# Optimization experiments

Measured on AMD Instinct MI355X. Metric: run time of the kernel, lower is better.

The kernel has to match this reference:

```python
import jax, jax.numpy as jnp
import numpy as np

N = 16384
D = 512
K = 1024          # fixed num_clusters (torch code uses randint(2, N//2))
NUM_ITERS = 10    # kmeans Lloyd iterations
NUM_CLUSTER_ITERS = 1
TEMPERATURE = 0.1
CONCENTRATION = 0.1
EPS = 1e-6


def setup_inputs() -> dict:
    key = jax.random.key(0)
    feats = jax.random.normal(key, (N, D), dtype=jnp.float32)
    return {"feats": feats}


def _assign(feats, centroids, x_sq):
    c_sq = jnp.sum(centroids * centroids, axis=-1)            # [K]
    d = x_sq[:, None] - 2.0 * (feats @ centroids.T) + c_sq[None, :]
    return jnp.argmin(d, axis=-1)                             # [N] int32


def _kmeans(feats, num_clusters, num_iters):
    x_sq = jnp.sum(feats * feats, axis=-1)                    # [N]
    init_centroids = feats[:num_clusters]                     # deterministic init

    def body(_, centroids):
        clusters = _assign(feats, centroids, x_sq)
        sums = jax.ops.segment_sum(feats, clusters, num_segments=num_clusters)
        counts = jax.ops.segment_sum(jnp.ones((feats.shape[0],), feats.dtype),
                                     clusters, num_segments=num_clusters)
        new_c = sums / jnp.maximum(counts, 1.0)[:, None]
        # keep old centroid for empty clusters
        return jnp.where(counts[:, None] > 0, new_c, centroids)

    centroids = jax.lax.fori_loop(0, num_iters, body, init_centroids)
    clusters = _assign(feats, centroids, x_sq)
    counts = jax.ops.segment_sum(jnp.ones((feats.shape[0],), feats.dtype),
                                 clusters, num_segments=num_clusters)
    return clusters, centroids, counts


def reference(feats):
    clusters, centroids, _ = _kmeans(feats, K, NUM_ITERS)
    # per-point squared residuals gathered by cluster id, scatter-added to [K, D]
    resid2 = (feats - centroids[clusters]) ** 2               # [N, D]
    dists = jax.ops.segment_sum(resid2, clusters, num_segments=K)  # [K, D]
    # entropy loss branch (concentration phi)
    p = jnp.exp(-dists / CONCENTRATION)
    Q = p / jnp.sum(p)
    entropy = jnp.mean(Q * jnp.log(Q + EPS)) / NUM_CLUSTER_ITERS
    # nll branch (temperature t)
    p2 = jnp.exp(-dists / TEMPERATURE)
    nll = -jnp.mean(jnp.log(p2 + EPS))
    return entropy + nll
```

## Files before the change

### kernel.cpp

```cpp
#include <hip/hip_runtime.h>
#include <math.h>

#define N 16384
#define D 512
#define K 1024
#define NUM_ITERS 10
#define TEMPERATURE 0.1f
#define CONCENTRATION 0.1f
#define EPS 1e-6f

typedef unsigned short ushort_t;
typedef unsigned int uint_t;
typedef unsigned long long u64;
typedef __attribute__((ext_vector_type(4))) float floatx4;
typedef __attribute__((ext_vector_type(8))) short shortx8;

__device__ inline ushort_t f2h(float f) {
    _Float16 h = (_Float16)f;
    return *(ushort_t*)&h;
}

__device__ inline unsigned ford(float f) {
    unsigned b = __float_as_uint(f);
    return (b & 0x80000000u) ? ~b : (b | 0x80000000u);
}

__device__ inline void f4add(float4& a, const float4& b) {
    a.x += b.x; a.y += b.y; a.z += b.z; a.w += b.w;
}

__device__ inline void gld16(const void* g, void* l) {
    __builtin_amdgcn_global_load_lds(
        (const __attribute__((address_space(1))) void*)(uintptr_t)(g),
        (__attribute__((address_space(3))) void*)(uintptr_t)(l), 16, 0, 0);
}

#define WAITVM(n_lit) asm volatile("s_waitcnt vmcnt(" #n_lit ")" ::: "memory")

__global__ void split_kernel(const float* __restrict__ x, ushort_t* __restrict__ hi,
                             u64* __restrict__ best2, int n4) {
    int i = blockIdx.x * 256 + threadIdx.x;
    if (i >= n4) return;
    float4 v = ((const float4*)x)[i];
    ushort4 hv = {f2h(v.x), f2h(v.y), f2h(v.z), f2h(v.w)};
    ((ushort4*)hi)[i] = hv;
    if (i < 2 * N) best2[i] = ~0ull;
}

__global__ void rowsq_kernel(const float* __restrict__ x, float* __restrict__ out, int rows) {
    int row = blockIdx.x * 4 + (threadIdx.x >> 6);
    int lane = threadIdx.x & 63;
    if (row >= rows) return;
    const float* r = x + (size_t)row * D;
    float s = 0.f;
    for (int i = lane; i < D; i += 64) { float v = r[i]; s += v * v; }
    for (int off = 32; off > 0; off >>= 1) s += __shfl_down(s, off, 64);
    if (lane == 0) out[row] = s;
}

__global__ __launch_bounds__(512, 2) void assign_mfma2(
    const ushort_t* __restrict__ Ah, const ushort_t* __restrict__ Bh,
    const float* __restrict__ csq, u64* __restrict__ best)
{
    __shared__ __align__(16) ushort_t sA[4][8192];
    __shared__ __align__(16) ushort_t sB[4][8192];

    const int tid = threadIdx.x;
    const int lane = tid & 63;
    const int wave = tid >> 6;
    const int wr = wave >> 2, wc = wave & 3;
    const int quad = lane >> 4, l16 = lane & 15;

    const int bid = (int)blockIdx.x;
    const int xid = bid & 7;
    const int s = bid >> 3;
    const int brow = (xid << 3) + (s >> 2);
    const int bcol = s & 3;
    const int row0 = brow * 256, col0 = bcol * 256;

    floatx4 acc[8][4];
#pragma unroll
    for (int a = 0; a < 8; ++a)
#pragma unroll
        for (int b = 0; b < 4; ++b) acc[a][b] = (floatx4){0.f, 0.f, 0.f, 0.f};

    const int swz = (quad ^ (l16 & 3) ^ ((l16 >> 2) & 3)) * 8;
    const int aoff = (wr * 128 + l16) * 32 + swz;
    const int boff = (wc * 64 + l16) * 32 + swz;

    auto stage = [&](int h) {
        const int u_h = h >> 2;
        const int part = h & 3;
        const int kh = part >> 1;
        const int reg = ((u_h & 1) << 1) | kh;
        const int d_off = u_h * 64 + kh * 32;
        const ushort_t* src = (part & 1) ? Bh : Ah;
        const int r0 = (part & 1) ? col0 : row0;
        ushort_t* dstreg = (part & 1) ? &sB[reg][0] : &sA[reg][0];
#pragma unroll
        for (int ii = 0; ii < 2; ++ii) {
            const int idx = ii * 512 + tid;
            const int row = idx >> 2;
            const int kb = (idx & 3) ^ (row & 3) ^ ((row >> 2) & 3);
            gld16(src + (size_t)(r0 + row) * D + d_off + kb * 8, dstreg + idx * 8);
        }
    };

    #pragma unroll
    for (int h = 0; h < 6; ++h) stage(h);
    WAITVM(8);
    __builtin_amdgcn_s_barrier();
    __builtin_amdgcn_sched_barrier(0);

    shortx8 fb[4];
#pragma unroll
    for (int u = 0; u < 8; ++u) {
        const int rbase = (u & 1) << 1;
#pragma unroll
        for (int p = 0; p < 4; ++p) {
            const int g = u * 4 + p;
            if (g + 6 < 32) stage(g + 6);
            const int kh = p >> 1;
            const int ih = p & 1;
            const ushort_t* Areg = &sA[rbase + kh][0];
            const ushort_t* Breg = &sB[rbase + kh][0];
            shortx8 fa[4];
            if (ih == 0) {
#pragma unroll
                for (int j = 0; j < 4; ++j) fb[j] = *(const shortx8*)&Breg[boff + j * 512];
            }
#pragma unroll
            for (int i = 0; i < 4; ++i) fa[i] = *(const shortx8*)&Areg[aoff + (ih * 4 + i) * 512];
            __builtin_amdgcn_s_setprio(1);
#pragma unroll
            for (int i = 0; i < 4; ++i)
#pragma unroll
                for (int j = 0; j < 4; ++j)
                    acc[ih * 4 + i][j] = __builtin_amdgcn_mfma_f32_16x16x32_f16(
                        fa[i], fb[j], acc[ih * 4 + i][j], 0, 0, 0);
            __builtin_amdgcn_s_setprio(0);
            if ((p == 1 || p == 3) && !(u == 7 && p == 3)) {
                asm volatile("s_waitcnt lgkmcnt(0)" ::: "memory");
                if (u == 7 && p == 1)      { WAITVM(0); }
                else if (u == 6 && p == 3) { WAITVM(4); }
                else                       { WAITVM(8); }
                __builtin_amdgcn_s_barrier();
                __builtin_amdgcn_sched_barrier(0);
            }
        }
    }

    float csqv[4];
#pragma unroll
    for (int j = 0; j < 4; ++j) csqv[j] = csq[col0 + wc * 64 + j * 16 + l16];

    const int k0 = col0 + wc * 64 + l16;
#pragma unroll
    for (int i = 0; i < 8; ++i) {
#pragma unroll
        for (int r = 0; r < 4; ++r) {
            float bv = csqv[0] - 2.0f * acc[i][0][r];
            int bk = k0;
#pragma unroll
            for (int j = 1; j < 4; ++j) {
                float v = csqv[j] - 2.0f * acc[i][j][r];
                int kk = k0 + j * 16;
                if (v < bv || (v == bv && kk < bk)) { bv = v; bk = kk; }
            }
#pragma unroll
            for (int m = 1; m < 16; m <<= 1) {
                float ov = __shfl_xor(bv, m, 64);
                int ok = __shfl_xor(bk, m, 64);
                if (ov < bv || (ov == bv && ok < bk)) { bv = ov; bk = ok; }
            }
            if (l16 == 0) {
                int p = row0 + wr * 128 + i * 16 + quad * 4 + r;
                u64 pk = ((u64)ford(bv) << 32) | (unsigned)bk;
                atomicMin(&best[p], pk);
            }
        }
    }
}

#define CU_WAVES 8
#define CHUNKS (N / 128)
#define ROUNDS 4
#define WIN (CHUNKS / ROUNDS)
#define CPW (WIN / CU_WAVES)
#define KPB 2

__global__ __launch_bounds__(512) void cluster_update(
    const float* __restrict__ feats, const u64* __restrict__ best,
    u64* __restrict__ best_other,
    float* __restrict__ cent, ushort_t* __restrict__ Bh,
    float* __restrict__ csq)
{
    __shared__ int list[KPB][CU_WAVES][CPW * 128];
    __shared__ int lcnt[KPB][CU_WAVES];
    __shared__ float4 part[CU_WAVES][64][2];
    __shared__ int pcnt_s[CU_WAVES];

    const int tid = threadIdx.x;
    const int lane = tid & 63;
    const int wave = tid >> 6;
    const int kbase = (int)blockIdx.x * KPB;

    float4 a0[KPB], a1[KPB];
    int cnttot[KPB];
#pragma unroll
    for (int q = 0; q < KPB; ++q) {
        a0[q] = (float4){0.f, 0.f, 0.f, 0.f};
        a1[q] = (float4){0.f, 0.f, 0.f, 0.f};
        cnttot[q] = 0;
    }

    for (int round = 0; round < ROUNDS; ++round) {
        int cw[KPB];
#pragma unroll
        for (int q = 0; q < KPB; ++q) cw[q] = 0;
#pragma unroll
        for (int cc = 0; cc < CPW; ++cc) {
            int chunk = round * WIN + wave * CPW + cc;
            ulonglong2 v = ((const ulonglong2*)best)[chunk * 64 + lane];
            int id0 = (int)(uint_t)v.x;
            int id1 = (int)(uint_t)v.y;
            int p0 = chunk * 128 + 2 * lane;
            u64 lanem = (1ull << lane) - 1ull;
#pragma unroll
            for (int q = 0; q < KPB; ++q) {
                const int kq = kbase + q;
                u64 m0 = __ballot(id0 == kq);
                u64 m1 = __ballot(id1 == kq);
                int c0 = __popcll(m0);
                if (id0 == kq) list[q][wave][cw[q] + __popcll(m0 & lanem)] = p0;
                if (id1 == kq) list[q][wave][cw[q] + c0 + __popcll(m1 & lanem)] = p0 + 1;
                cw[q] += c0 + __popcll(m1);
            }
        }
#pragma unroll
        for (int q = 0; q < KPB; ++q) {
            if (lane == 0) lcnt[q][wave] = cw[q];
            cnttot[q] += cw[q];
        }
        __syncthreads();

#pragma unroll
        for (int q = 0; q < KPB; ++q) {
            int off[CU_WAVES]; int T = 0;
#pragma unroll
            for (int j = 0; j < CU_WAVES; ++j) { off[j] = T; T += lcnt[q][j]; }

            for (int g0 = wave; g0 < T; g0 += CU_WAVES * 4) {
                int nb = 0; int pidx[4];
#pragma unroll
                for (int b = 0; b < 4; ++b) {
                    int g = g0 + CU_WAVES * b;
                    if (g < T) {
                        int j = 0;
#pragma unroll
                        for (int jj = 1; jj < CU_WAVES; ++jj) if (g >= off[jj]) j = jj;
                        pidx[nb++] = list[q][j][g - off[j]];
                    }
                }
                float4 x[4][2];
#pragma unroll
                for (int b = 0; b < 4; ++b) if (b < nb) {
                    const float4* r = (const float4*)(feats + (size_t)pidx[b] * D) + lane * 2;
                    x[b][0] = r[0]; x[b][1] = r[1];
                }
#pragma unroll
                for (int b = 0; b < 4; ++b) if (b < nb) {
                    f4add(a0[q], x[b][0]); f4add(a1[q], x[b][1]);
                }
            }
        }
        __syncthreads();
    }

#pragma unroll
    for (int q = 0; q < KPB; ++q) {
        const int k = kbase + q;
        part[wave][lane][0] = a0[q]; part[wave][lane][1] = a1[q];
        if (lane == 0) pcnt_s[wave] = cnttot[q];
        __syncthreads();

        if (wave == 0) {
            float4 s0 = part[0][lane][0], s1 = part[0][lane][1];
            int c = pcnt_s[0];
#pragma unroll
            for (int w = 1; w < CU_WAVES; ++w) {
                f4add(s0, part[w][lane][0]); f4add(s1, part[w][lane][1]);
                c += pcnt_s[w];
            }

            float4* crow = (float4*)(cent + (size_t)k * D) + lane * 2;
            float4 c0, c1;
            if (c > 0) {
                float cf = (float)c;
                c0 = (float4){s0.x / cf, s0.y / cf, s0.z / cf, s0.w / cf};
                c1 = (float4){s1.x / cf, s1.y / cf, s1.z / cf, s1.w / cf};
            } else {
                c0 = crow[0]; c1 = crow[1];
            }
            crow[0] = c0; crow[1] = c1;

            ushort4 hv;
            hv.x = f2h(c0.x); hv.y = f2h(c0.y); hv.z = f2h(c0.z); hv.w = f2h(c0.w);
            ((ushort4*)(Bh + (size_t)k * D))[lane * 2] = hv;
            hv.x = f2h(c1.x); hv.y = f2h(c1.y); hv.z = f2h(c1.z); hv.w = f2h(c1.w);
            ((ushort4*)(Bh + (size_t)k * D))[lane * 2 + 1] = hv;

            float s = c0.x * c0.x + c0.y * c0.y + c0.z * c0.z + c0.w * c0.w
                    + c1.x * c1.x + c1.y * c1.y + c1.z * c1.z + c1.w * c1.w;
            for (int o = 32; o > 0; o >>= 1) s += __shfl_xor(s, o, 64);
            if (lane == 0) csq[k] = s;
        }
        __syncthreads();
    }

    if (tid < 16 * KPB) best_other[(size_t)blockIdx.x * 16 * KPB + tid] = ~0ull;
}

__global__ __launch_bounds__(512) void dist_gather(
    const float* __restrict__ feats, const float* __restrict__ cent,
    const u64* __restrict__ best, float* __restrict__ dists)
{
    __shared__ int list[KPB][CU_WAVES][CPW * 128];
    __shared__ int lcnt[KPB][CU_WAVES];
    __shared__ float4 part[CU_WAVES][64][2];

    const int tid = threadIdx.x;
    const int lane = tid & 63;
    const int wave = tid >> 6;
    const int kbase = (int)blockIdx.x * KPB;

    float4 c0[KPB], c1[KPB];
#pragma unroll
    for (int q = 0; q < KPB; ++q) {
        const float4* crow = (const float4*)(cent + (size_t)(kbase + q) * D) + lane * 2;
        c0[q] = crow[0]; c1[q] = crow[1];
    }

    float4 a0[KPB], a1[KPB];
#pragma unroll
    for (int q = 0; q < KPB; ++q) {
        a0[q] = (float4){0.f, 0.f, 0.f, 0.f};
        a1[q] = (float4){0.f, 0.f, 0.f, 0.f};
    }

    for (int round = 0; round < ROUNDS; ++round) {
        int cw[KPB];
#pragma unroll
        for (int q = 0; q < KPB; ++q) cw[q] = 0;
#pragma unroll
        for (int cc = 0; cc < CPW; ++cc) {
            int chunk = round * WIN + wave * CPW + cc;
            ulonglong2 v = ((const ulonglong2*)best)[chunk * 64 + lane];
            int id0 = (int)(uint_t)v.x;
            int id1 = (int)(uint_t)v.y;
            int p0 = chunk * 128 + 2 * lane;
            u64 lanem = (1ull << lane) - 1ull;
#pragma unroll
            for (int q = 0; q < KPB; ++q) {
                const int kq = kbase + q;
                u64 m0 = __ballot(id0 == kq);
                u64 m1 = __ballot(id1 == kq);
                int cc0 = __popcll(m0);
                if (id0 == kq) list[q][wave][cw[q] + __popcll(m0 & lanem)] = p0;
                if (id1 == kq) list[q][wave][cw[q] + cc0 + __popcll(m1 & lanem)] = p0 + 1;
                cw[q] += cc0 + __popcll(m1);
            }
        }
#pragma unroll
        for (int q = 0; q < KPB; ++q) {
            if (lane == 0) lcnt[q][wave] = cw[q];
        }
        __syncthreads();

#pragma unroll
        for (int q = 0; q < KPB; ++q) {
            int off[CU_WAVES]; int T = 0;
#pragma unroll
            for (int j = 0; j < CU_WAVES; ++j) { off[j] = T; T += lcnt[q][j]; }

            for (int g0 = wave; g0 < T; g0 += CU_WAVES * 4) {
                int nb = 0; int pidx[4];
#pragma unroll
                for (int b = 0; b < 4; ++b) {
                    int g = g0 + CU_WAVES * b;
                    if (g < T) {
                        int j = 0;
#pragma unroll
                        for (int jj = 1; jj < CU_WAVES; ++jj) if (g >= off[jj]) j = jj;
                        pidx[nb++] = list[q][j][g - off[j]];
                    }
                }
                float4 x[4][2];
#pragma unroll
                for (int b = 0; b < 4; ++b) if (b < nb) {
                    const float4* r = (const float4*)(feats + (size_t)pidx[b] * D) + lane * 2;
                    x[b][0] = r[0]; x[b][1] = r[1];
                }
#pragma unroll
                for (int b = 0; b < 4; ++b) if (b < nb) {
                    float r;
                    r = x[b][0].x - c0[q].x; a0[q].x += r * r;  r = x[b][0].y - c0[q].y; a0[q].y += r * r;
                    r = x[b][0].z - c0[q].z; a0[q].z += r * r;  r = x[b][0].w - c0[q].w; a0[q].w += r * r;
                    r = x[b][1].x - c1[q].x; a1[q].x += r * r;  r = x[b][1].y - c1[q].y; a1[q].y += r * r;
                    r = x[b][1].z - c1[q].z; a1[q].z += r * r;  r = x[b][1].w - c1[q].w; a1[q].w += r * r;
                }
            }
        }
        __syncthreads();
    }

#pragma unroll
    for (int q = 0; q < KPB; ++q) {
        part[wave][lane][0] = a0[q]; part[wave][lane][1] = a1[q];
        __syncthreads();
        if (wave == 0) {
            float4 s0 = part[0][lane][0], s1 = part[0][lane][1];
#pragma unroll
            for (int w = 1; w < CU_WAVES; ++w) { f4add(s0, part[w][lane][0]); f4add(s1, part[w][lane][1]); }
            float4* drow = (float4*)(dists + (size_t)(kbase + q) * D) + lane * 2;
            drow[0] = s0; drow[1] = s1;
        }
        __syncthreads();
    }
}

__global__ void sump_kernel(const float* __restrict__ dists, double* __restrict__ S) {
    int tid = threadIdx.x;
    float v = 0.f;
    for (int idx = blockIdx.x * 256 + tid; idx < K * D; idx += 256 * 256)
        v += expf(-(dists[idx] / CONCENTRATION));
    __shared__ float red[4];
    for (int off = 32; off > 0; off >>= 1) v += __shfl_down(v, off, 64);
    if ((tid & 63) == 0) red[tid >> 6] = v;
    __syncthreads();
    if (tid == 0) atomicAdd(S, (double)(red[0] + red[1] + red[2] + red[3]));
}

__global__ void loss_kernel(const float* __restrict__ dists, const double* __restrict__ Sd,
                            double* __restrict__ acc2) {
    int tid = threadIdx.x;
    float S = (float)Sd[0];
    float e = 0.f, nl = 0.f;
    for (int idx = blockIdx.x * 256 + tid; idx < K * D; idx += 256 * 256) {
        float dv = dists[idx];
        float p = expf(-(dv / CONCENTRATION));
        float qq = p / S;
        e += qq * logf(qq + EPS);
        float p2 = expf(-(dv / TEMPERATURE));
        nl += logf(p2 + EPS);
    }
    __shared__ float rede[4];
    __shared__ float redn[4];
    for (int off = 32; off > 0; off >>= 1) { e += __shfl_down(e, off, 64); nl += __shfl_down(nl, off, 64); }
    if ((tid & 63) == 0) { rede[tid >> 6] = e; redn[tid >> 6] = nl; }
    __syncthreads();
    if (tid == 0) {
        atomicAdd(&acc2[0], (double)(rede[0] + rede[1] + rede[2] + rede[3]));
        atomicAdd(&acc2[1], (double)(redn[0] + redn[1] + redn[2] + redn[3]));
    }
}

__global__ void finalize_kernel(const double* __restrict__ acc2, float* __restrict__ out) {
    double kd = (double)(K * D);
    double entropy = acc2[0] / kd;
    double nll = -(acc2[1] / kd);
    out[0] = (float)(entropy + nll);
}

extern "C" void kernel_launch(void* const* d_in, const int* in_sizes, int n_in,
                              void* d_out, int out_size, void* d_ws, size_t ws_size,
                              hipStream_t stream) {
    const float* feats = (const float*)d_in[0];
    float* out = (float*)d_out;

    ushort_t* Ah = (ushort_t*)d_ws;
    ushort_t* Bh = Ah + (size_t)N * D;
    float* centroids = (float*)(Bh + (size_t)K * D);
    float* dists     = centroids + (size_t)K * D;
    float* csq       = dists + (size_t)K * D;
    u64*   best0     = (u64*)(csq + K);
    u64*   best1     = best0 + N;
    double* scal     = (double*)(best1 + N);

    split_kernel<<<(N * D / 4) / 256, 256, 0, stream>>>(feats, Ah, best0, N * D / 4);
    hipMemcpyAsync(centroids, feats, (size_t)K * D * sizeof(float),
                   hipMemcpyDeviceToDevice, stream);
    rowsq_kernel<<<K / 4, 256, 0, stream>>>(feats, csq, K);

    for (int it = 0; it < NUM_ITERS; ++it) {
        u64* cur = (it & 1) ? best1 : best0;
        u64* oth = (it & 1) ? best0 : best1;
        const ushort_t* bh = (it == 0) ? Ah : Bh;
        assign_mfma2<<<(N / 256) * (K / 256), 512, 0, stream>>>(Ah, bh, csq, cur);
        cluster_update<<<K / KPB, 512, 0, stream>>>(feats, cur, oth, centroids, Bh, csq);
    }
    u64* fin = (NUM_ITERS & 1) ? best1 : best0;
    assign_mfma2<<<(N / 256) * (K / 256), 512, 0, stream>>>(Ah, Bh, csq, fin);

    dist_gather<<<K / KPB, 512, 0, stream>>>(feats, centroids, fin, dists);

    hipMemsetAsync(scal, 0, 3 * sizeof(double), stream);
    sump_kernel<<<256, 256, 0, stream>>>(dists, &scal[0]);
    loss_kernel<<<256, 256, 0, stream>>>(dists, &scal[0], &scal[1]);
    finalize_kernel<<<1, 1, 0, stream>>>(&scal[1], out);
}
```

Measured before the change: 739.3 us.

## Fuse k-means iterations into one persistent cooperative kernel with grid syncs

Result: slower. 2.242 ms (+203.3%).

```diff
diff --git a/kernel.cpp b/kernel.cpp
--- a/kernel.cpp
+++ b/kernel.cpp
@@ -1,5 +1,8 @@
 #include <hip/hip_runtime.h>
+#include <hip/hip_cooperative_groups.h>
 #include <math.h>
+
+namespace cg = cooperative_groups;
 
 #define N 16384
 #define D 512
@@ -58,374 +61,383 @@
     if (lane == 0) out[row] = s;
 }
 
-__global__ __launch_bounds__(512, 2) void assign_mfma2(
-    const ushort_t* __restrict__ Ah, const ushort_t* __restrict__ Bh,
-    const float* __restrict__ csq, u64* __restrict__ best)
+#define CU_WAVES 8
+#define CHUNKS (N / 128)
+#define ROUNDS 4
+#define WIN (CHUNKS / ROUNDS)
+#define CPW (WIN / CU_WAVES)
+#define KPB 4
+
+__global__ __launch_bounds__(512, 2) void kmeans_fused(
+    const ushort_t* __restrict__ Ah, ushort_t* Bh, float* csq,
+    u64* best0, u64* best1, const float* __restrict__ feats,
+    float* cent, float* dists)
 {
-    __shared__ __align__(16) ushort_t sA[4][8192];
-    __shared__ __align__(16) ushort_t sB[4][8192];
+    cg::grid_group grid = cg::this_grid();
+    __shared__ __align__(16) unsigned char smem[131072];
 
     const int tid = threadIdx.x;
     const int lane = tid & 63;
     const int wave = tid >> 6;
-    const int wr = wave >> 2, wc = wave & 3;
-    const int quad = lane >> 4, l16 = lane & 15;
-
     const int bid = (int)blockIdx.x;
+
     const int xid = bid & 7;
     const int s = bid >> 3;
     const int brow = (xid << 3) + (s >> 2);
     const int bcol = s & 3;
     const int row0 = brow * 256, col0 = bcol * 256;
 
-    floatx4 acc[8][4];
-#pragma unroll
-    for (int a = 0; a < 8; ++a)
-#pragma unroll
-        for (int b = 0; b < 4; ++b) acc[a][b] = (floatx4){0.f, 0.f, 0.f, 0.f};
+    const int wr = wave >> 2, wc = wave & 3;
+    const int quad = lane >> 4, l16 = lane & 15;
+
+    ushort_t* sA = (ushort_t*)smem;
+    ushort_t* sB = (ushort_t*)(smem + 65536);
 
     const int swz = (quad ^ (l16 & 3) ^ ((l16 >> 2) & 3)) * 8;
     const int aoff = (wr * 128 + l16) * 32 + swz;
     const int boff = (wc * 64 + l16) * 32 + swz;
 
-    auto stage = [&](int h) {
-        const int u_h = h >> 2;
-        const int part = h & 3;
-        const int kh = part >> 1;
-        const int reg = ((u_h & 1) << 1) | kh;
-        const int d_off = u_h * 64 + kh * 32;
-        const ushort_t* src = (part & 1) ? Bh : Ah;
-        const int r0 = (part & 1) ? col0 : row0;
-        ushort_t* dstreg = (part & 1) ? &sB[reg][0] : &sA[reg][0];
-#pragma unroll
-        for (int ii = 0; ii < 2; ++ii) {
-            const int idx = ii * 512 + tid;
-            const int row = idx >> 2;
-            const int kb = (idx & 3) ^ (row & 3) ^ ((row >> 2) & 3);
-            gld16(src + (size_t)(r0 + row) * D + d_off + kb * 8, dstreg + idx * 8);
+    const int kbase = bid * KPB;
+
+#pragma unroll 1
+    for (int it = 0; it <= NUM_ITERS; ++it) {
+        const ushort_t* Bp = (it == 0) ? Ah : Bh;
+        u64* cur = (it & 1) ? best1 : best0;
+        u64* oth = (it & 1) ? best0 : best1;
+
+        {
+            floatx4 acc[8][4];
+#pragma unroll
+            for (int a = 0; a < 8; ++a)
+#pragma unroll
+                for (int b = 0; b < 4; ++b) acc[a][b] = (floatx4){0.f, 0.f, 0.f, 0.f};
+
+            auto stage = [&](int h) {
+                const int u_h = h >> 2;
+                const int part = h & 3;
+                const int kh = part >> 1;
+                const int reg = ((u_h & 1) << 1) | kh;
+                const int d_off = u_h * 64 + kh * 32;
+                const ushort_t* src = (part & 1) ? Bp : Ah;
+                const int r0 = (part & 1) ? col0 : row0;
+                ushort_t* dstreg = ((part & 1) ? sB : sA) + reg * 8192;
+#pragma unroll
+                for (int ii = 0; ii < 2; ++ii) {
+                    const int idx = ii * 512 + tid;
+                    const int row = idx >> 2;
+                    const int kb = (idx & 3) ^ (row & 3) ^ ((row >> 2) & 3);
+                    gld16(src + (size_t)(r0 + row) * D + d_off + kb * 8, dstreg + idx * 8);
+                }
+            };
+
+#pragma unroll
+            for (int h = 0; h < 6; ++h) stage(h);
+            WAITVM(8);
+            __builtin_amdgcn_s_barrier();
+            __builtin_amdgcn_sched_barrier(0);
+
+            shortx8 fb[4];
+#pragma unroll
+            for (int u = 0; u < 8; ++u) {
+                const int rbase = (u & 1) << 1;
+#pragma unroll
+                for (int p = 0; p < 4; ++p) {
+                    const int g = u * 4 + p;
+                    if (g + 6 < 32) stage(g + 6);
+                    const int kh = p >> 1;
+                    const int ih = p & 1;
+                    const ushort_t* Areg = sA + (rbase + kh) * 8192;
+                    const ushort_t* Breg = sB + (rbase + kh) * 8192;
+                    shortx8 fa[4];
+                    if (ih == 0) {
+#pragma unroll
+                        for (int j = 0; j < 4; ++j) fb[j] = *(const shortx8*)&Breg[boff + j * 512];
+                    }
+#pragma unroll
+                    for (int i = 0; i < 4; ++i) fa[i] = *(const shortx8*)&Areg[aoff + (ih * 4 + i) * 512];
+                    __builtin_amdgcn_s_setprio(1);
+#pragma unroll
+                    for (int i = 0; i < 4; ++i)
+#pragma unroll
+                        for (int j = 0; j < 4; ++j)
+                            acc[ih * 4 + i][j] = __builtin_amdgcn_mfma_f32_16x16x32_f16(
+                                fa[i], fb[j], acc[ih * 4 + i][j], 0, 0, 0);
+                    __builtin_amdgcn_s_setprio(0);
+                    if ((p == 1 || p == 3) && !(u == 7 && p == 3)) {
+                        asm volatile("s_waitcnt lgkmcnt(0)" ::: "memory");
+                        if (u == 7 && p == 1)      { WAITVM(0); }
+                        else if (u == 6 && p == 3) { WAITVM(4); }
+                        else                       { WAITVM(8); }
+                        __builtin_amdgcn_s_barrier();
+                        __builtin_amdgcn_sched_barrier(0);
+                    }
+                }
+            }
+
+            float csqv[4];
+#pragma unroll
+            for (int j = 0; j < 4; ++j) csqv[j] = csq[col0 + wc * 64 + j * 16 + l16];
+
+            const int k0 = col0 + wc * 64 + l16;
+#pragma unroll
+            for (int i = 0; i < 8; ++i) {
+#pragma unroll
+                for (int r = 0; r < 4; ++r) {
+                    float bv = csqv[0] - 2.0f * acc[i][0][r];
+                    int bk = k0;
+#pragma unroll
+                    for (int j = 1; j < 4; ++j) {
+                        float v = csqv[j] - 2.0f * acc[i][j][r];
+                        int kk = k0 + j * 16;
+                        if (v < bv || (v == bv && kk < bk)) { bv = v; bk = kk; }
+                    }
+#pragma unroll
+                    for (int m = 1; m < 16; m <<= 1) {
+                        float ov = __shfl_xor(bv, m, 64);
+                        int ok = __shfl_xor(bk, m, 64);
+                        if (ov < bv || (ov == bv && ok < bk)) { bv = ov; bk = ok; }
+                    }
+                    if (l16 == 0) {
+                        int p = row0 + wr * 128 + i * 16 + quad * 4 + r;
+                        u64 pk = ((u64)ford(bv) << 32) | (unsigned)bk;
+                        atomicMin(&cur[p], pk);
+                    }
+                }
+            }
         }
-    };
-
-    #pragma unroll
-    for (int h = 0; h < 6; ++h) stage(h);
-    WAITVM(8);
-    __builtin_amdgcn_s_barrier();
-    __builtin_amdgcn_sched_barrier(0);
-
-    shortx8 fb[4];
-#pragma unroll
-    for (int u = 0; u < 8; ++u) {
-        const int rbase = (u & 1) << 1;
-#pragma unroll
-        for (int p = 0; p < 4; ++p) {
-            const int g = u * 4 + p;
-            if (g + 6 < 32) stage(g + 6);
-            const int kh = p >> 1;
-            const int ih = p & 1;
-            const ushort_t* Areg = &sA[rbase + kh][0];
-            const ushort_t* Breg = &sB[rbase + kh][0];
-            shortx8 fa[4];
-            if (ih == 0) {
-#pragma unroll
-                for (int j = 0; j < 4; ++j) fb[j] = *(const shortx8*)&Breg[boff + j * 512];
-            }
-#pragma unroll
-            for (int i = 0; i < 4; ++i) fa[i] = *(const shortx8*)&Areg[aoff + (ih * 4 + i) * 512];
-            __builtin_amdgcn_s_setprio(1);
-#pragma unroll
-            for (int i = 0; i < 4; ++i)
-#pragma unroll
-                for (int j = 0; j < 4; ++j)
-                    acc[ih * 4 + i][j] = __builtin_amdgcn_mfma_f32_16x16x32_f16(
-                        fa[i], fb[j], acc[ih * 4 + i][j], 0, 0, 0);
-            __builtin_amdgcn_s_setprio(0);
-            if ((p == 1 || p == 3) && !(u == 7 && p == 3)) {
-                asm volatile("s_waitcnt lgkmcnt(0)" ::: "memory");
-                if (u == 7 && p == 1)      { WAITVM(0); }
-                else if (u == 6 && p == 3) { WAITVM(4); }
-                else                       { WAITVM(8); }
-                __builtin_amdgcn_s_barrier();
-                __builtin_amdgcn_sched_barrier(0);
-            }
+        __threadfence();
+        grid.sync();
+
+        if (it < NUM_ITERS) {
+            int* list = (int*)smem;
+            int* lcnt = (int*)(smem + 65536);
+            int* pcnt = (int*)(smem + 65536 + 128);
+            float4* part = (float4*)(smem + 65536 + 256);
+
+            float4 a0[KPB], a1[KPB];
+            int cnttot[KPB];
+#pragma unroll
+            for (int q = 0; q < KPB; ++q) {
+                a0[q] = (float4){0.f, 0.f, 0.f, 0.f};
+                a1[q] = (float4){0.f, 0.f, 0.f, 0.f};
+                cnttot[q] = 0;
+            }
+
+            for (int round = 0; round < ROUNDS; ++round) {
+                int cw[KPB];
+#pragma unroll
+                for (int q = 0; q < KPB; ++q) cw[q] = 0;
+#pragma unroll
+                for (int cc = 0; cc < CPW; ++cc) {
+                    int chunk = round * WIN + wave * CPW + cc;
+                    ulonglong2 v = ((const ulonglong2*)cur)[chunk * 64 + lane];
+                    int id0 = (int)(uint_t)v.x;
+                    int id1 = (int)(uint_t)v.y;
+                    int p0 = chunk * 128 + 2 * lane;
+                    u64 lanem = (1ull << lane) - 1ull;
+#pragma unroll
+                    for (int q = 0; q < KPB; ++q) {
+                        const int kq = kbase + q;
+                        u64 m0 = __ballot(id0 == kq);
+                        u64 m1 = __ballot(id1 == kq);
+                        int c0n = __popcll(m0);
+                        if (id0 == kq) list[(q * 8 + wave) * 512 + cw[q] + __popcll(m0 & lanem)] = p0;
+                        if (id1 == kq) list[(q * 8 + wave) * 512 + cw[q] + c0n + __popcll(m1 & lanem)] = p0 + 1;
+                        cw[q] += c0n + __popcll(m1);
+                    }
+                }
+#pragma unroll
+                for (int q = 0; q < KPB; ++q) {
+                    if (lane == 0) lcnt[q * 8 + wave] = cw[q];
+                    cnttot[q] += cw[q];
+                }
+                __syncthreads();
+
+#pragma unroll
+                for (int q = 0; q < KPB; ++q) {
+                    int off[CU_WAVES]; int T = 0;
+#pragma unroll
+                    for (int j = 0; j < CU_WAVES; ++j) { off[j] = T; T += lcnt[q * 8 + j]; }
+
+                    for (int g0 = wave; g0 < T; g0 += CU_WAVES * 4) {
+                        int nb = 0; int pidx[4];
+#pragma unroll
+                        for (int b = 0; b < 4; ++b) {
+                            int g = g0 + CU_WAVES * b;
+                            if (g < T) {
+                                int j = 0;
+#pragma unroll
+                                for (int jj = 1; jj < CU_WAVES; ++jj) if (g >= off[jj]) j = jj;
+                                pidx[nb++] = list[(q * 8 + j) * 512 + (g - off[j])];
+                            }
+                        }
+                        float4 x[4][2];
+#pragma unroll
+                        for (int b = 0; b < 4; ++b) if (b < nb) {
+                            const float4* r = (const float4*)(feats + (size_t)pidx[b] * D) + lane * 2;
+                            x[b][0] = r[0]; x[b][1] = r[1];
+                        }
+#pragma unroll
+                        for (int b = 0; b < 4; ++b) if (b < nb) {
+                            f4add(a0[q], x[b][0]); f4add(a1[q], x[b][1]);
+                        }
+                    }
+                }
+                __syncthreads();
+            }
+
+#pragma unroll
+            for (int q = 0; q < KPB; ++q) {
+                const int k = kbase + q;
+                part[(wave * 64 + lane) * 2 + 0] = a0[q];
+                part[(wave * 64 + lane) * 2 + 1] = a1[q];
+                if (lane == 0) pcnt[wave] = cnttot[q];
+                __syncthreads();
+
+                if (wave == 0) {
+                    float4 s0 = part[(0 * 64 + lane) * 2 + 0], s1 = part[(0 * 64 + lane) * 2 + 1];
+                    int c = pcnt[0];
+#pragma unroll
+                    for (int w = 1; w < CU_WAVES; ++w) {
+                        f4add(s0, part[(w * 64 + lane) * 2 + 0]);
+                        f4add(s1, part[(w * 64 + lane) * 2 + 1]);
+                        c += pcnt[w];
+                    }
+
+                    float4* crow = (float4*)(cent + (size_t)k * D) + lane * 2;
+                    float4 c0, c1;
+                    if (c > 0) {
+                        float cf = (float)c;
+                        c0 = (float4){s0.x / cf, s0.y / cf, s0.z / cf, s0.w / cf};
+                        c1 = (float4){s1.x / cf, s1.y / cf, s1.z / cf, s1.w / cf};
+                    } else {
+                        c0 = crow[0]; c1 = crow[1];
+                    }
+                    crow[0] = c0; crow[1] = c1;
+
+                    ushort4 hv;
+                    hv.x = f2h(c0.x); hv.y = f2h(c0.y); hv.z = f2h(c0.z); hv.w = f2h(c0.w);
+                    ((ushort4*)(Bh + (size_t)k * D))[lane * 2] = hv;
+                    hv.x = f2h(c1.x); hv.y = f2h(c1.y); hv.z = f2h(c1.z); hv.w = f2h(c1.w);
+                    ((ushort4*)(Bh + (size_t)k * D))[lane * 2 + 1] = hv;
+
+                    float sq = c0.x * c0.x + c0.y * c0.y + c0.z * c0.z + c0.w * c0.w
+                             + c1.x * c1.x + c1.y * c1.y + c1.z * c1.z + c1.w * c1.w;
+                    for (int o = 32; o > 0; o >>= 1) sq += __shfl_xor(sq, o, 64);
+                    if (lane == 0) csq[k] = sq;
+                }
+                __syncthreads();
+            }
+
+            if (tid < 16 * KPB) oth[(size_t)bid * 16 * KPB + tid] = ~0ull;
+            __threadfence();
+            grid.sync();
         }
     }
 
-    float csqv[4];
-#pragma unroll
-    for (int j = 0; j < 4; ++j) csqv[j] = csq[col0 + wc * 64 + j * 16 + l16];
-
-    const int k0 = col0 + wc * 64 + l16;
-#pragma unroll
-    for (int i = 0; i < 8; ++i) {
-#pragma unroll
-        for (int r = 0; r < 4; ++r) {
-            float bv = csqv[0] - 2.0f * acc[i][0][r];
-            int bk = k0;
-#pragma unroll
-            for (int j = 1; j < 4; ++j) {
-                float v = csqv[j] - 2.0f * acc[i][j][r];
-                int kk = k0 + j * 16;
-                if (v < bv || (v == bv && kk < bk)) { bv = v; bk = kk; }
-            }
-#pragma unroll
-            for (int m = 1; m < 16; m <<= 1) {
-                float ov = __shfl_xor(bv, m, 64);
-                int ok = __shfl_xor(bk, m, 64);
-                if (ov < bv || (ov == bv && ok < bk)) { bv = ov; bk = ok; }
-            }
-            if (l16 == 0) {
-                int p = row0 + wr * 128 + i * 16 + quad * 4 + r;
-                u64 pk = ((u64)ford(bv) << 32) | (unsigned)bk;
-                atomicMin(&best[p], pk);
-            }
+    {
+        u64* fin = best0;
+        int* list = (int*)smem;
+        int* lcnt = (int*)(smem + 65536);
+        float4* part = (float4*)(smem + 65536 + 256);
+
+        float4 c0q[KPB], c1q[KPB];
+#pragma unroll
+        for (int q = 0; q < KPB; ++q) {
+            const float4* crow = (const float4*)(cent + (size_t)(kbase + q) * D) + lane * 2;
+            c0q[q] = crow[0]; c1q[q] = crow[1];
         }
-    }
-}
-
-#define CU_WAVES 8
-#define CHUNKS (N / 128)
-#define ROUNDS 4
-#define WIN (CHUNKS / ROUNDS)
-#define CPW (WIN / CU_WAVES)
-#define KPB 2
-
-__global__ __launch_bounds__(512) void cluster_update(
-    const float* __restrict__ feats, const u64* __restrict__ best,
-    u64* __restrict__ best_other,
-    float* __restrict__ cent, ushort_t* __restrict__ Bh,
-    float* __restrict__ csq)
-{
-    __shared__ int list[KPB][CU_WAVES][CPW * 128];
-    __shared__ int lcnt[KPB][CU_WAVES];
-    __shared__ float4 part[CU_WAVES][64][2];
-    __shared__ int pcnt_s[CU_WAVES];
-
-    const int tid = threadIdx.x;
-    const int lane = tid & 63;
-    const int wave = tid >> 6;
-    const int kbase = (int)blockIdx.x * KPB;
-
-    float4 a0[KPB], a1[KPB];
-    int cnttot[KPB];
-#pragma unroll
-    for (int q = 0; q < KPB; ++q) {
-        a0[q] = (float4){0.f, 0.f, 0.f, 0.f};
-        a1[q] = (float4){0.f, 0.f, 0.f, 0.f};
-        cnttot[q] = 0;
-    }
-
-    for (int round = 0; round < ROUNDS; ++round) {
-        int cw[KPB];
-#pragma unroll
-        for (int q = 0; q < KPB; ++q) cw[q] = 0;
-#pragma unroll
-        for (int cc = 0; cc < CPW; ++cc) {
-            int chunk = round * WIN + wave * CPW + cc;
-            ulonglong2 v = ((const ulonglong2*)best)[chunk * 64 + lane];
-            int id0 = (int)(uint_t)v.x;
-            int id1 = (int)(uint_t)v.y;
-            int p0 = chunk * 128 + 2 * lane;
-            u64 lanem = (1ull << lane) - 1ull;
+
+        float4 a0[KPB], a1[KPB];
+#pragma unroll
+        for (int q = 0; q < KPB; ++q) {
+            a0[q] = (float4){0.f, 0.f, 0.f, 0.f};
+            a1[q] = (float4){0.f, 0.f, 0.f, 0.f};
+        }
+
+        for (int round = 0; round < ROUNDS; ++round) {
+            int cw[KPB];
+#pragma unroll
+            for (int q = 0; q < KPB; ++q) cw[q] = 0;
+#pragma unroll
+            for (int cc = 0; cc < CPW; ++cc) {
+                int chunk = round * WIN + wave * CPW + cc;
+                ulonglong2 v = ((const ulonglong2*)fin)[chunk * 64 + lane];
+                int id0 = (int)(uint_t)v.x;
+                int id1 = (int)(uint_t)v.y;
+                int p0 = chunk * 128 + 2 * lane;
+                u64 lanem = (1ull << lane) - 1ull;
+#pragma unroll
+                for (int q = 0; q < KPB; ++q) {
+                    const int kq = kbase + q;
+                    u64 m0 = __ballot(id0 == kq);
+                    u64 m1 = __ballot(id1 == kq);
+                    int c0n = __popcll(m0);
+                    if (id0 == kq) list[(q * 8 + wave) * 512 + cw[q] + __popcll(m0 & lanem)] = p0;
+                    if (id1 == kq) list[(q * 8 + wave) * 512 + cw[q] + c0n + __popcll(m1 & lanem)] = p0 + 1;
+                    cw[q] += c0n + __popcll(m1);
+                }
+            }
 #pragma unroll
             for (int q = 0; q < KPB; ++q) {
-                const int kq = kbase + q;
-                u64 m0 = __ballot(id0 == kq);
-                u64 m1 = __ballot(id1 == kq);
-                int c0 = __popcll(m0);
-                if (id0 == kq) list[q][wave][cw[q] + __popcll(m0 & lanem)] = p0;
-                if (id1 == kq) list[q][wave][cw[q] + c0 + __popcll(m1 & lanem)] = p0 + 1;
-                cw[q] += c0 + __popcll(m1);
-            }
+                if (lane == 0) lcnt[q * 8 + wave] = cw[q];
+            }
+            __syncthreads();
+
+#pragma unroll
+            for (int q = 0; q < KPB; ++q) {
+                int off[CU_WAVES]; int T = 0;
+#pragma unroll
+                for (int j = 0; j < CU_WAVES; ++j) { off[j] = T; T += lcnt[q * 8 + j]; }
+
+                for (int g0 = wave; g0 < T; g0 += CU_WAVES * 4) {
+                    int nb = 0; int pidx[4];
+#pragma unroll
+                    for (int b = 0; b < 4; ++b) {
+                        int g = g0 + CU_WAVES * b;
+                        if (g < T) {
+                            int j = 0;
+#pragma unroll
+                            for (int jj = 1; jj < CU_WAVES; ++jj) if (g >= off[jj]) j = jj;
+                            pidx[nb++] = list[(q * 8 + j) * 512 + (g - off[j])];
+                        }
+                    }
+                    float4 x[4][2];
+#pragma unroll
+                    for (int b = 0; b < 4; ++b) if (b < nb) {
+                        const float4* r = (const float4*)(feats + (size_t)pidx[b] * D) + lane * 2;
+                        x[b][0] = r[0]; x[b][1] = r[1];
+                    }
+#pragma unroll
+                    for (int b = 0; b < 4; ++b) if (b < nb) {
+                        float rr;
+                        rr = x[b][0].x - c0q[q].x; a0[q].x += rr * rr;  rr = x[b][0].y - c0q[q].y; a0[q].y += rr * rr;
+                        rr = x[b][0].z - c0q[q].z; a0[q].z += rr * rr;  rr = x[b][0].w - c0q[q].w; a0[q].w += rr * rr;
+                        rr = x[b][1].x - c1q[q].x; a1[q].x += rr * rr;  rr = x[b][1].y - c1q[q].y; a1[q].y += rr * rr;
+                        rr = x[b][1].z - c1q[q].z; a1[q].z += rr * rr;  rr = x[b][1].w - c1q[q].w; a1[q].w += rr * rr;
+                    }
+                }
+            }
+            __syncthreads();
         }
+
 #pragma unroll
         for (int q = 0; q < KPB; ++q) {
-            if (lane == 0) lcnt[q][wave] = cw[q];
-            cnttot[q] += cw[q];
+            part[(wave * 64 + lane) * 2 + 0] = a0[q];
+            part[(wave * 64 + lane) * 2 + 1] = a1[q];
+            __syncthreads();
+            if (wave == 0) {
+                float4 s0 = part[(0 * 64 + lane) * 2 + 0], s1 = part[(0 * 64 + lane) * 2 + 1];
+#pragma unroll
+                for (int w = 1; w < CU_WAVES; ++w) {
+                    f4add(s0, part[(w * 64 + lane) * 2 + 0]);
+                    f4add(s1, part[(w * 64 + lane) * 2 + 1]);
+                }
+                float4* drow = (float4*)(dists + (size_t)(kbase + q) * D) + lane * 2;
+                drow[0] = s0; drow[1] = s1;
+            }
+            __syncthreads();
         }
-        __syncthreads();
-
-#pragma unroll
-        for (int q = 0; q < KPB; ++q) {
-            int off[CU_WAVES]; int T = 0;
-#pragma unroll
-            for (int j = 0; j < CU_WAVES; ++j) { off[j] = T; T += lcnt[q][j]; }
-
-            for (int g0 = wave; g0 < T; g0 += CU_WAVES * 4) {
-                int nb = 0; int pidx[4];
-#pragma unroll
-                for (int b = 0; b < 4; ++b) {
-                    int g = g0 + CU_WAVES * b;
-                    if (g < T) {
-                        int j = 0;
-#pragma unroll
-                        for (int jj = 1; jj < CU_WAVES; ++jj) if (g >= off[jj]) j = jj;
-                        pidx[nb++] = list[q][j][g - off[j]];
-                    }
-                }
-                float4 x[4][2];
-#pragma unroll
-                for (int b = 0; b < 4; ++b) if (b < nb) {
-                    const float4* r = (const float4*)(feats + (size_t)pidx[b] * D) + lane * 2;
-                    x[b][0] = r[0]; x[b][1] = r[1];
-                }
-#pragma unroll
-                for (int b = 0; b < 4; ++b) if (b < nb) {
-                    f4add(a0[q], x[b][0]); f4add(a1[q], x[b][1]);
-                }
-            }
-        }
-        __syncthreads();
-    }
-
-#pragma unroll
-    for (int q = 0; q < KPB; ++q) {
-        const int k = kbase + q;
-        part[wave][lane][0] = a0[q]; part[wave][lane][1] = a1[q];
-        if (lane == 0) pcnt_s[wave] = cnttot[q];
-        __syncthreads();
-
-        if (wave == 0) {
-            float4 s0 = part[0][lane][0], s1 = part[0][lane][1];
-            int c = pcnt_s[0];
-#pragma unroll
-            for (int w = 1; w < CU_WAVES; ++w) {
-                f4add(s0, part[w][lane][0]); f4add(s1, part[w][lane][1]);
-                c += pcnt_s[w];
-            }
-
-            float4* crow = (float4*)(cent + (size_t)k * D) + lane * 2;
-            float4 c0, c1;
-            if (c > 0) {
-                float cf = (float)c;
-                c0 = (float4){s0.x / cf, s0.y / cf, s0.z / cf, s0.w / cf};
-                c1 = (float4){s1.x / cf, s1.y / cf, s1.z / cf, s1.w / cf};
-            } else {
-                c0 = crow[0]; c1 = crow[1];
-            }
-            crow[0] = c0; crow[1] = c1;
-
-            ushort4 hv;
-            hv.x = f2h(c0.x); hv.y = f2h(c0.y); hv.z = f2h(c0.z); hv.w = f2h(c0.w);
-            ((ushort4*)(Bh + (size_t)k * D))[lane * 2] = hv;
-            hv.x = f2h(c1.x); hv.y = f2h(c1.y); hv.z = f2h(c1.z); hv.w = f2h(c1.w);
-            ((ushort4*)(Bh + (size_t)k * D))[lane * 2 + 1] = hv;
-
-            float s = c0.x * c0.x + c0.y * c0.y + c0.z * c0.z + c0.w * c0.w
-                    + c1.x * c1.x + c1.y * c1.y + c1.z * c1.z + c1.w * c1.w;
-            for (int o = 32; o > 0; o >>= 1) s += __shfl_xor(s, o, 64);
-            if (lane == 0) csq[k] = s;
-        }
-        __syncthreads();
-    }
-
-    if (tid < 16 * KPB) best_other[(size_t)blockIdx.x * 16 * KPB + tid] = ~0ull;
-}
-
-__global__ __launch_bounds__(512) void dist_gather(
-    const float* __restrict__ feats, const float* __restrict__ cent,
-    const u64* __restrict__ best, float* __restrict__ dists)
-{
-    __shared__ int list[KPB][CU_WAVES][CPW * 128];
-    __shared__ int lcnt[KPB][CU_WAVES];
-    __shared__ float4 part[CU_WAVES][64][2];
-
-    const int tid = threadIdx.x;
-    const int lane = tid & 63;
-    const int wave = tid >> 6;
-    const int kbase = (int)blockIdx.x * KPB;
-
-    float4 c0[KPB], c1[KPB];
-#pragma unroll
-    for (int q = 0; q < KPB; ++q) {
-        const float4* crow = (const float4*)(cent + (size_t)(kbase + q) * D) + lane * 2;
-        c0[q] = crow[0]; c1[q] = crow[1];
-    }
-
-    float4 a0[KPB], a1[KPB];
-#pragma unroll
-    for (int q = 0; q < KPB; ++q) {
-        a0[q] = (float4){0.f, 0.f, 0.f, 0.f};
-        a1[q] = (float4){0.f, 0.f, 0.f, 0.f};
-    }
-
-    for (int round = 0; round < ROUNDS; ++round) {
-        int cw[KPB];
-#pragma unroll
-        for (int q = 0; q < KPB; ++q) cw[q] = 0;
-#pragma unroll
-        for (int cc = 0; cc < CPW; ++cc) {
-            int chunk = round * WIN + wave * CPW + cc;
-            ulonglong2 v = ((const ulonglong2*)best)[chunk * 64 + lane];
-            int id0 = (int)(uint_t)v.x;
-            int id1 = (int)(uint_t)v.y;
-            int p0 = chunk * 128 + 2 * lane;
-            u64 lanem = (1ull << lane) - 1ull;
-#pragma unroll
-            for (int q = 0; q < KPB; ++q) {
-                const int kq = kbase + q;
-                u64 m0 = __ballot(id0 == kq);
-                u64 m1 = __ballot(id1 == kq);
-                int cc0 = __popcll(m0);
-                if (id0 == kq) list[q][wave][cw[q] + __popcll(m0 & lanem)] = p0;
-                if (id1 == kq) list[q][wave][cw[q] + cc0 + __popcll(m1 & lanem)] = p0 + 1;
-                cw[q] += cc0 + __popcll(m1);
-            }
-        }
-#pragma unroll
-        for (int q = 0; q < KPB; ++q) {
-            if (lane == 0) lcnt[q][wave] = cw[q];
-        }
-        __syncthreads();
-
-#pragma unroll
-        for (int q = 0; q < KPB; ++q) {
-            int off[CU_WAVES]; int T = 0;
-#pragma unroll
-            for (int j = 0; j < CU_WAVES; ++j) { off[j] = T; T += lcnt[q][j]; }
-
-            for (int g0 = wave; g0 < T; g0 += CU_WAVES * 4) {
-                int nb = 0; int pidx[4];
-#pragma unroll
-                for (int b = 0; b < 4; ++b) {
-                    int g = g0 + CU_WAVES * b;
-                    if (g < T) {
-                        int j = 0;
-#pragma unroll
-                        for (int jj = 1; jj < CU_WAVES; ++jj) if (g >= off[jj]) j = jj;
-                        pidx[nb++] = list[q][j][g - off[j]];
-                    }
-                }
-                float4 x[4][2];
-#pragma unroll
-                for (int b = 0; b < 4; ++b) if (b < nb) {
-                    const float4* r = (const float4*)(feats + (size_t)pidx[b] * D) + lane * 2;
-                    x[b][0] = r[0]; x[b][1] = r[1];
-                }
-#pragma unroll
-                for (int b = 0; b < 4; ++b) if (b < nb) {
-                    float r;
-                    r = x[b][0].x - c0[q].x; a0[q].x += r * r;  r = x[b][0].y - c0[q].y; a0[q].y += r * r;
-                    r = x[b][0].z - c0[q].z; a0[q].z += r * r;  r = x[b][0].w - c0[q].w; a0[q].w += r * r;
-                    r = x[b][1].x - c1[q].x; a1[q].x += r * r;  r = x[b][1].y - c1[q].y; a1[q].y += r * r;
-                    r = x[b][1].z - c1[q].z; a1[q].z += r * r;  r = x[b][1].w - c1[q].w; a1[q].w += r * r;
-                }
-            }
-        }
-        __syncthreads();
-    }
-
-#pragma unroll
-    for (int q = 0; q < KPB; ++q) {
-        part[wave][lane][0] = a0[q]; part[wave][lane][1] = a1[q];
-        __syncthreads();
-        if (wave == 0) {
-            float4 s0 = part[0][lane][0], s1 = part[0][lane][1];
-#pragma unroll
-            for (int w = 1; w < CU_WAVES; ++w) { f4add(s0, part[w][lane][0]); f4add(s1, part[w][lane][1]); }
-            float4* drow = (float4*)(dists + (size_t)(kbase + q) * D) + lane * 2;
-            drow[0] = s0; drow[1] = s1;
-        }
-        __syncthreads();
     }
 }
 
@@ -492,17 +504,21 @@
                    hipMemcpyDeviceToDevice, stream);
     rowsq_kernel<<<K / 4, 256, 0, stream>>>(feats, csq, K);
 
-    for (int it = 0; it < NUM_ITERS; ++it) {
-        u64* cur = (it & 1) ? best1 : best0;
-        u64* oth = (it & 1) ? best0 : best1;
-        const ushort_t* bh = (it == 0) ? Ah : Bh;
-        assign_mfma2<<<(N / 256) * (K / 256), 512, 0, stream>>>(Ah, bh, csq, cur);
-        cluster_update<<<K / KPB, 512, 0, stream>>>(feats, cur, oth, centroids, Bh, csq);
+    {
+        const ushort_t* AhArg = Ah;
+        ushort_t* BhArg = Bh;
+        float* csqArg = csq;
+        u64* b0Arg = best0;
+        u64* b1Arg = best1;
+        const float* featsArg = feats;
+        float* centArg = centroids;
+        float* distsArg = dists;
+        void* kargs[] = {(void*)&AhArg, (void*)&BhArg, (void*)&csqArg,
+                         (void*)&b0Arg, (void*)&b1Arg, (void*)&featsArg,
+                         (void*)&centArg, (void*)&distsArg};
+        hipLaunchCooperativeKernel((const void*)kmeans_fused, dim3(256), dim3(512),
+                                   kargs, 0, stream);
     }
-    u64* fin = (NUM_ITERS & 1) ? best1 : best0;
-    assign_mfma2<<<(N / 256) * (K / 256), 512, 0, stream>>>(Ah, Bh, csq, fin);
-
-    dist_gather<<<K / KPB, 512, 0, stream>>>(feats, centroids, fin, dists);
 
     hipMemsetAsync(scal, 0, 3 * sizeof(double), stream);
     sump_kernel<<<256, 256, 0, stream>>>(dists, &scal[0]);
```
